# Optimization experiments

Hardware: AMD Instinct MI355X
Metric: run time of the kernel (lower is better)

Reference implementation:

```python
import jax, jax.numpy as jnp
from jax import lax
import numpy as np

I, H = 2048, 128
EPS = 1e-5


def setup_inputs() -> dict:
    key = jax.random.key(0)
    ks = jax.random.split(key, 12)
    s_ih = 1.0 / np.sqrt(H)  # torch nn.RNN init: U(-1/sqrt(H), 1/sqrt(H))
    s_fc = 1.0 / np.sqrt(H)
    u = lambda k, shape, s: jax.random.uniform(k, shape, jnp.float32, -s, s)
    return {
        "x": jax.random.normal(ks[0], (64, 512, I), jnp.float32),
        "W_ih": u(ks[1], (H, I), s_ih),
        "b_ih": u(ks[2], (H,), s_ih),
        "W_hh": u(ks[3], (H, H), s_ih),
        "b_hh": u(ks[4], (H,), s_ih),
        "W1": u(ks[5], (H, H), s_fc),
        "b1": u(ks[6], (H,), s_fc),
        "W2": u(ks[7], (H, H), s_fc),
        "b2": u(ks[8], (H,), s_fc),
        "gamma": jnp.ones((H,), jnp.float32),
        "beta": jnp.zeros((H,), jnp.float32),
    }


def reference(x, W_ih, b_ih, W_hh, b_hh, W1, b1, W2, b2, gamma, beta):
    B = x.shape[0]
    # Precompute input projection for all timesteps: [B, T, H]
    xp = jnp.einsum('bti,hi->bth', x, W_ih) + b_ih

    def step(h, xt):  # h: [B, H], xt: [B, H]
        h_new = jnp.tanh(xt + h @ W_hh.T + b_hh)
        return h_new, None

    h0 = jnp.zeros((B, H), x.dtype)
    hT, _ = lax.scan(step, h0, jnp.swapaxes(xp, 0, 1))  # scan over T

    z = jax.nn.relu(hT @ W1.T + b1)
    z = jax.nn.relu(z @ W2.T + b2)
    mu = jnp.mean(z, axis=-1, keepdims=True)
    var = jnp.mean(jnp.square(z - mu), axis=-1, keepdims=True)
    return gamma * (z - mu) * lax.rsqrt(var + EPS) + beta
```

## Files before the change

### kernel.cpp

```cpp
#include <hip/hip_runtime.h>


typedef __bf16 bf16x8 __attribute__((ext_vector_type(8)));
typedef float  f32x4  __attribute__((ext_vector_type(4)));

#define T_STEPS 512
#define I_DIM   2048
#define H_DIM   128
#define B_DIM   64
#define M_TOT   (B_DIM * T_STEPS)

__device__ __forceinline__ unsigned short f2bf(float f) {
    unsigned int u = __float_as_uint(f);
    u += 0x7FFFu + ((u >> 16) & 1u);
    return (unsigned short)(u >> 16);
}

#define BM  128
#define BK  64
#define LDK 72

__global__ __launch_bounds__(256) void gemm_xp(
    const float* __restrict__ x,
    const float* __restrict__ w,
    const float* __restrict__ b_ih,
    const float* __restrict__ b_hh,
    float* __restrict__ xp)
{
    __shared__ __align__(16) unsigned short As[BM * LDK];
    __shared__ __align__(16) unsigned short Bs[H_DIM * LDK];

    const int tid = threadIdx.x;
    const int m0  = blockIdx.x * BM;

    const int r0 = tid >> 4;
    const int c4 = tid & 15;

    const int lane = tid & 63;
    const int wave = tid >> 6;
    const int wm   = (wave >> 1) * 64;
    const int wn   = (wave & 1) * 64;
    const int l16  = lane & 15;
    const int quad = lane >> 4;

    f32x4 acc[4][4] = {};

    float4 ar[8], br[8];

    auto load_tiles = [&](int k0) {
        #pragma unroll
        for (int i = 0; i < 8; ++i)
            ar[i] = *(const float4*)(x + (size_t)(m0 + i * 16 + r0) * I_DIM + k0 + c4 * 4);
        #pragma unroll
        for (int i = 0; i < 8; ++i)
            br[i] = *(const float4*)(w + (size_t)(i * 16 + r0) * I_DIM + k0 + c4 * 4);
    };

    auto store_tiles = [&]() {
        #pragma unroll
        for (int i = 0; i < 8; ++i) {
            ushort4 v;
            v.x = f2bf(ar[i].x); v.y = f2bf(ar[i].y);
            v.z = f2bf(ar[i].z); v.w = f2bf(ar[i].w);
            *(ushort4*)(As + (i * 16 + r0) * LDK + c4 * 4) = v;
        }
        #pragma unroll
        for (int i = 0; i < 8; ++i) {
            ushort4 v;
            v.x = f2bf(br[i].x); v.y = f2bf(br[i].y);
            v.z = f2bf(br[i].z); v.w = f2bf(br[i].w);
            *(ushort4*)(Bs + (i * 16 + r0) * LDK + c4 * 4) = v;
        }
    };

    load_tiles(0);

    for (int k0 = 0; k0 < I_DIM; k0 += BK) {
        __syncthreads();
        store_tiles();
        if (k0 + BK < I_DIM) load_tiles(k0 + BK);
        __syncthreads();

        #pragma unroll
        for (int kt = 0; kt < 2; ++kt) {
            bf16x8 af[4], bfr[4];
            #pragma unroll
            for (int i = 0; i < 4; ++i)
                af[i] = *(const bf16x8*)(As + (wm + i * 16 + l16) * LDK + kt * 32 + quad * 8);
            #pragma unroll
            for (int i = 0; i < 4; ++i)
                bfr[i] = *(const bf16x8*)(Bs + (wn + i * 16 + l16) * LDK + kt * 32 + quad * 8);
            #pragma unroll
            for (int i = 0; i < 4; ++i)
                #pragma unroll
                for (int j = 0; j < 4; ++j)
                    acc[i][j] = __builtin_amdgcn_mfma_f32_16x16x32_bf16(af[i], bfr[j], acc[i][j], 0, 0, 0);
        }
    }

    #pragma unroll
    for (int j = 0; j < 4; ++j) {
        const int col  = wn + j * 16 + l16;
        const float bias = b_ih[col] + b_hh[col];
        #pragma unroll
        for (int i = 0; i < 4; ++i) {
            #pragma unroll
            for (int r = 0; r < 4; ++r) {
                const int row = wm + i * 16 + quad * 4 + r;
                xp[(size_t)(m0 + row) * H_DIM + col] = acc[i][j][r] + bias;
            }
        }
    }
}

__global__ __launch_bounds__(256) void rnn_tail(
    const float* __restrict__ xp,
    const float* __restrict__ Whh,
    const float* __restrict__ W1, const float* __restrict__ b1,
    const float* __restrict__ W2, const float* __restrict__ b2,
    const float* __restrict__ gamma, const float* __restrict__ beta,
    float* __restrict__ out)
{
    __shared__ float hs[2][H_DIM];
    __shared__ float zb[H_DIM];
    __shared__ float red[4][2];

    const int tid  = threadIdx.x;
    const int b    = blockIdx.x;
    const int j    = tid >> 1;
    const int half = tid & 1;

    float4 wr[16];
    {
        const float4* wrow = (const float4*)(Whh + j * H_DIM + half * 64);
        #pragma unroll
        for (int i = 0; i < 16; ++i) wr[i] = wrow[i];
    }

    if (tid < H_DIM) hs[0][tid] = 0.f;
    const float* xpp = xp + (size_t)b * T_STEPS * H_DIM;
    float xv = xpp[j];
    __syncthreads();

    for (int t = 0; t < T_STEPS; ++t) {
        float xnext = (t < T_STEPS - 1) ? xpp[(t + 1) * H_DIM + j] : 0.f;

        const float4* hv = (const float4*)(hs[t & 1] + half * 64);
        float p0 = 0.f, p1 = 0.f, p2 = 0.f, p3 = 0.f;
        #pragma unroll
        for (int i = 0; i < 16; i += 4) {
            float4 h0 = hv[i], h1 = hv[i + 1], h2 = hv[i + 2], h3 = hv[i + 3];
            p0 += wr[i].x     * h0.x + wr[i].y     * h0.y + wr[i].z     * h0.z + wr[i].w     * h0.w;
            p1 += wr[i + 1].x * h1.x + wr[i + 1].y * h1.y + wr[i + 1].z * h1.z + wr[i + 1].w * h1.w;
            p2 += wr[i + 2].x * h2.x + wr[i + 2].y * h2.y + wr[i + 2].z * h2.z + wr[i + 2].w * h2.w;
            p3 += wr[i + 3].x * h3.x + wr[i + 3].y * h3.y + wr[i + 3].z * h3.z + wr[i + 3].w * h3.w;
        }
        float p = (p0 + p1) + (p2 + p3);
        p += __shfl_xor(p, 1);

        float a  = xv + p;
        float e  = __expf(-2.f * fabsf(a));
        float th = (1.f - e) / (1.f + e);
        th = copysignf(th, a);

        if (half == 0) hs[(t + 1) & 1][j] = th;
        xv = xnext;
        __syncthreads();
    }

    {
        const float4* wv = (const float4*)(W1 + j * H_DIM + half * 64);
        const float4* hv = (const float4*)(hs[0] + half * 64);
        float p0 = 0.f, p1 = 0.f;
        #pragma unroll
        for (int i = 0; i < 16; i += 2) {
            float4 w0 = wv[i], w1_ = wv[i + 1], h0 = hv[i], h1 = hv[i + 1];
            p0 += w0.x * h0.x + w0.y * h0.y + w0.z * h0.z + w0.w * h0.w;
            p1 += w1_.x * h1.x + w1_.y * h1.y + w1_.z * h1.z + w1_.w * h1.w;
        }
        float p = p0 + p1;
        p += __shfl_xor(p, 1);
        float z = fmaxf(p + b1[j], 0.f);
        if (half == 0) zb[j] = z;
    }
    __syncthreads();

    {
        const float4* wv = (const float4*)(W2 + j * H_DIM + half * 64);
        const float4* zv = (const float4*)(zb + half * 64);
        float p0 = 0.f, p1 = 0.f;
        #pragma unroll
        for (int i = 0; i < 16; i += 2) {
            float4 w0 = wv[i], w1_ = wv[i + 1], z0 = zv[i], z1 = zv[i + 1];
            p0 += w0.x * z0.x + w0.y * z0.y + w0.z * z0.z + w0.w * z0.w;
            p1 += w1_.x * z1.x + w1_.y * z1.y + w1_.z * z1.z + w1_.w * z1.w;
        }
        float p = p0 + p1;
        p += __shfl_xor(p, 1);
        float z2 = fmaxf(p + b2[j], 0.f);
        if (half == 0) hs[1][j] = z2;
    }
    __syncthreads();

    float v = (tid < H_DIM) ? hs[1][tid] : 0.f;
    float s = v, q = v * v;
    #pragma unroll
    for (int o = 1; o < 64; o <<= 1) {
        s += __shfl_xor(s, o);
        q += __shfl_xor(q, o);
    }
    const int lane = tid & 63, wave = tid >> 6;
    if (lane == 0) { red[wave][0] = s; red[wave][1] = q; }
    __syncthreads();
    float S = red[0][0] + red[1][0] + red[2][0] + red[3][0];
    float Q = red[0][1] + red[1][1] + red[2][1] + red[3][1];
    float mu   = S * (1.f / 128.f);
    float var  = Q * (1.f / 128.f) - mu * mu;
    float rstd = rsqrtf(var + 1e-5f);
    if (tid < H_DIM)
        out[b * H_DIM + tid] = gamma[tid] * (v - mu) * rstd + beta[tid];
}

extern "C" void kernel_launch(void* const* d_in, const int* in_sizes, int n_in,
                              void* d_out, int out_size, void* d_ws, size_t ws_size,
                              hipStream_t stream) {
    const float* x     = (const float*)d_in[0];
    const float* W_ih  = (const float*)d_in[1];
    const float* b_ih  = (const float*)d_in[2];
    const float* W_hh  = (const float*)d_in[3];
    const float* b_hh  = (const float*)d_in[4];
    const float* W1    = (const float*)d_in[5];
    const float* b1    = (const float*)d_in[6];
    const float* W2    = (const float*)d_in[7];
    const float* b2    = (const float*)d_in[8];
    const float* gamma = (const float*)d_in[9];
    const float* beta  = (const float*)d_in[10];
    float* out = (float*)d_out;

    float* xp = (float*)d_ws;

    gemm_xp<<<dim3(M_TOT / BM), dim3(256), 0, stream>>>(x, W_ih, b_ih, b_hh, xp);
    rnn_tail<<<dim3(B_DIM), dim3(256), 0, stream>>>(xp, W_hh, W1, b1, W2, b2,
                                                    gamma, beta, out);
}
```

Measured before the change: 654.9 us.

## Batch 16 sequences per block and run recurrent matvec on bf16 MFMA

```diff
diff --git a/kernel.cpp b/kernel.cpp
--- a/kernel.cpp
+++ b/kernel.cpp
@@ -15,16 +15,27 @@
     u += 0x7FFFu + ((u >> 16) & 1u);
     return (unsigned short)(u >> 16);
 }
-
-#define BM  128
+__device__ __forceinline__ float bf2f(unsigned short u) {
+    return __uint_as_float(((unsigned int)u) << 16);
+}
+__device__ __forceinline__ bf16x8 packbf8(float4 lo, float4 hi) {
+    union { bf16x8 v; unsigned short u[8]; } r;
+    r.u[0] = f2bf(lo.x); r.u[1] = f2bf(lo.y); r.u[2] = f2bf(lo.z); r.u[3] = f2bf(lo.w);
+    r.u[4] = f2bf(hi.x); r.u[5] = f2bf(hi.y); r.u[6] = f2bf(hi.z); r.u[7] = f2bf(hi.w);
+    return r.v;
+}
+__device__ __forceinline__ float tanh_fast(float a) {
+    float q = __expf(a + a);
+    return (q - 1.f) * __builtin_amdgcn_rcpf(q + 1.f);
+}
+
+#define BM  64
 #define BK  64
 #define LDK 72
 
 __global__ __launch_bounds__(256) void gemm_xp(
-    const float* __restrict__ x,
-    const float* __restrict__ w,
-    const float* __restrict__ b_ih,
-    const float* __restrict__ b_hh,
+    const float* __restrict__ x, const float* __restrict__ w,
+    const float* __restrict__ b_ih, const float* __restrict__ b_hh,
     float* __restrict__ xp)
 {
     __shared__ __align__(16) unsigned short As[BM * LDK];
@@ -32,88 +43,79 @@
 
     const int tid = threadIdx.x;
     const int m0  = blockIdx.x * BM;
-
-    const int r0 = tid >> 4;
-    const int c4 = tid & 15;
-
-    const int lane = tid & 63;
-    const int wave = tid >> 6;
-    const int wm   = (wave >> 1) * 64;
-    const int wn   = (wave & 1) * 64;
-    const int l16  = lane & 15;
-    const int quad = lane >> 4;
-
-    f32x4 acc[4][4] = {};
-
-    float4 ar[8], br[8];
+    const int r0  = tid >> 4;
+    const int c4  = tid & 15;
+    const int lane = tid & 63, wave = tid >> 6;
+    const int wm = (wave >> 1) * 32;
+    const int wn = (wave & 1) * 64;
+    const int l16 = lane & 15, quad = lane >> 4;
+
+    f32x4 acc[2][4] = {};
+    float4 ar[4], br[8];
 
     auto load_tiles = [&](int k0) {
         #pragma unroll
-        for (int i = 0; i < 8; ++i)
+        for (int i = 0; i < 4; ++i)
             ar[i] = *(const float4*)(x + (size_t)(m0 + i * 16 + r0) * I_DIM + k0 + c4 * 4);
         #pragma unroll
         for (int i = 0; i < 8; ++i)
             br[i] = *(const float4*)(w + (size_t)(i * 16 + r0) * I_DIM + k0 + c4 * 4);
     };
-
     auto store_tiles = [&]() {
         #pragma unroll
+        for (int i = 0; i < 4; ++i) {
+            ushort4 v; v.x = f2bf(ar[i].x); v.y = f2bf(ar[i].y);
+                       v.z = f2bf(ar[i].z); v.w = f2bf(ar[i].w);
+            *(ushort4*)(As + (i * 16 + r0) * LDK + c4 * 4) = v;
+        }
+        #pragma unroll
         for (int i = 0; i < 8; ++i) {
-            ushort4 v;
-            v.x = f2bf(ar[i].x); v.y = f2bf(ar[i].y);
-            v.z = f2bf(ar[i].z); v.w = f2bf(ar[i].w);
-            *(ushort4*)(As + (i * 16 + r0) * LDK + c4 * 4) = v;
-        }
-        #pragma unroll
-        for (int i = 0; i < 8; ++i) {
-            ushort4 v;
-            v.x = f2bf(br[i].x); v.y = f2bf(br[i].y);
-            v.z = f2bf(br[i].z); v.w = f2bf(br[i].w);
+            ushort4 v; v.x = f2bf(br[i].x); v.y = f2bf(br[i].y);
+                       v.z = f2bf(br[i].z); v.w = f2bf(br[i].w);
             *(ushort4*)(Bs + (i * 16 + r0) * LDK + c4 * 4) = v;
         }
     };
 
     load_tiles(0);
-
     for (int k0 = 0; k0 < I_DIM; k0 += BK) {
         __syncthreads();
         store_tiles();
         if (k0 + BK < I_DIM) load_tiles(k0 + BK);
         __syncthreads();
-
         #pragma unroll
         for (int kt = 0; kt < 2; ++kt) {
-            bf16x8 af[4], bfr[4];
-            #pragma unroll
-            for (int i = 0; i < 4; ++i)
+            bf16x8 af[2], bfr[4];
+            #pragma unroll
+            for (int i = 0; i < 2; ++i)
                 af[i] = *(const bf16x8*)(As + (wm + i * 16 + l16) * LDK + kt * 32 + quad * 8);
             #pragma unroll
-            for (int i = 0; i < 4; ++i)
-                bfr[i] = *(const bf16x8*)(Bs + (wn + i * 16 + l16) * LDK + kt * 32 + quad * 8);
-            #pragma unroll
-            for (int i = 0; i < 4; ++i)
+            for (int j = 0; j < 4; ++j)
+                bfr[j] = *(const bf16x8*)(Bs + (wn + j * 16 + l16) * LDK + kt * 32 + quad * 8);
+            #pragma unroll
+            for (int i = 0; i < 2; ++i)
                 #pragma unroll
                 for (int j = 0; j < 4; ++j)
                     acc[i][j] = __builtin_amdgcn_mfma_f32_16x16x32_bf16(af[i], bfr[j], acc[i][j], 0, 0, 0);
         }
     }
-
     #pragma unroll
     for (int j = 0; j < 4; ++j) {
-        const int col  = wn + j * 16 + l16;
+        const int col = wn + j * 16 + l16;
         const float bias = b_ih[col] + b_hh[col];
         #pragma unroll
-        for (int i = 0; i < 4; ++i) {
+        for (int i = 0; i < 2; ++i)
             #pragma unroll
             for (int r = 0; r < 4; ++r) {
                 const int row = wm + i * 16 + quad * 4 + r;
                 xp[(size_t)(m0 + row) * H_DIM + col] = acc[i][j][r] + bias;
             }
-        }
-    }
-}
-
-__global__ __launch_bounds__(256) void rnn_tail(
+    }
+}
+
+#define NB  16
+#define LDH 136
+
+__global__ __launch_bounds__(256) void rnn_scan(
     const float* __restrict__ xp,
     const float* __restrict__ Whh,
     const float* __restrict__ W1, const float* __restrict__ b1,
@@ -121,104 +123,108 @@
     const float* __restrict__ gamma, const float* __restrict__ beta,
     float* __restrict__ out)
 {
-    __shared__ float hs[2][H_DIM];
-    __shared__ float zb[H_DIM];
-    __shared__ float red[4][2];
+    __shared__ __align__(16) unsigned short hbuf[2][NB * LDH];
+    __shared__ float ztmp[NB][129];
+    __shared__ float ztmp2[NB][129];
 
     const int tid  = threadIdx.x;
-    const int b    = blockIdx.x;
-    const int j    = tid >> 1;
-    const int half = tid & 1;
-
-    float4 wr[16];
-    {
-        const float4* wrow = (const float4*)(Whh + j * H_DIM + half * 64);
-        #pragma unroll
-        for (int i = 0; i < 16; ++i) wr[i] = wrow[i];
-    }
-
-    if (tid < H_DIM) hs[0][tid] = 0.f;
-    const float* xpp = xp + (size_t)b * T_STEPS * H_DIM;
-    float xv = xpp[j];
+    const int lane = tid & 63, w = tid >> 6;
+    const int l16  = lane & 15, quad = lane >> 4;
+    const int b0   = blockIdx.x * NB;
+
+    bf16x8 afr[2][4];
+    #pragma unroll
+    for (int t = 0; t < 2; ++t) {
+        const float* wrow = Whh + (32 * w + 16 * t + l16) * H_DIM;
+        #pragma unroll
+        for (int ks = 0; ks < 4; ++ks) {
+            float4 lo = *(const float4*)(wrow + 32 * ks + 8 * quad);
+            float4 hi = *(const float4*)(wrow + 32 * ks + 8 * quad + 4);
+            afr[t][ks] = packbf8(lo, hi);
+        }
+    }
+
+    const float* xpb = xp + (size_t)(b0 + l16) * T_STEPS * H_DIM + 32 * w + 4 * quad;
+    float4 xc0 = *(const float4*)(xpb);
+    float4 xc1 = *(const float4*)(xpb + 16);
+
+    for (int i = tid; i < NB * LDH; i += 256) hbuf[0][i] = 0;
     __syncthreads();
 
+    const f32x4 z4 = {0.f, 0.f, 0.f, 0.f};
+    const int rbase = l16 * LDH + quad * 8;
+
     for (int t = 0; t < T_STEPS; ++t) {
-        float xnext = (t < T_STEPS - 1) ? xpp[(t + 1) * H_DIM + j] : 0.f;
-
-        const float4* hv = (const float4*)(hs[t & 1] + half * 64);
-        float p0 = 0.f, p1 = 0.f, p2 = 0.f, p3 = 0.f;
-        #pragma unroll
-        for (int i = 0; i < 16; i += 4) {
-            float4 h0 = hv[i], h1 = hv[i + 1], h2 = hv[i + 2], h3 = hv[i + 3];
-            p0 += wr[i].x     * h0.x + wr[i].y     * h0.y + wr[i].z     * h0.z + wr[i].w     * h0.w;
-            p1 += wr[i + 1].x * h1.x + wr[i + 1].y * h1.y + wr[i + 1].z * h1.z + wr[i + 1].w * h1.w;
-            p2 += wr[i + 2].x * h2.x + wr[i + 2].y * h2.y + wr[i + 2].z * h2.z + wr[i + 2].w * h2.w;
-            p3 += wr[i + 3].x * h3.x + wr[i + 3].y * h3.y + wr[i + 3].z * h3.z + wr[i + 3].w * h3.w;
-        }
-        float p = (p0 + p1) + (p2 + p3);
-        p += __shfl_xor(p, 1);
-
-        float a  = xv + p;
-        float e  = __expf(-2.f * fabsf(a));
-        float th = (1.f - e) / (1.f + e);
-        th = copysignf(th, a);
-
-        if (half == 0) hs[(t + 1) & 1][j] = th;
-        xv = xnext;
+        const unsigned short* hb = hbuf[t & 1];
+        bf16x8 bf0 = *(const bf16x8*)(hb + rbase);
+        bf16x8 bf1 = *(const bf16x8*)(hb + rbase + 32);
+        bf16x8 bf2 = *(const bf16x8*)(hb + rbase + 64);
+        bf16x8 bf3 = *(const bf16x8*)(hb + rbase + 96);
+
+        const int tn = (t + 1 < T_STEPS) ? t + 1 : t;
+        float4 xn0 = *(const float4*)(xpb + (size_t)tn * H_DIM);
+        float4 xn1 = *(const float4*)(xpb + (size_t)tn * H_DIM + 16);
+
+        unsigned short* hn = hbuf[(t + 1) & 1];
+        #pragma unroll
+        for (int tl = 0; tl < 2; ++tl) {
+            f32x4 p0 = __builtin_amdgcn_mfma_f32_16x16x32_bf16(afr[tl][0], bf0, z4, 0, 0, 0);
+            p0 = __builtin_amdgcn_mfma_f32_16x16x32_bf16(afr[tl][1], bf1, p0, 0, 0, 0);
+            f32x4 p1 = __builtin_amdgcn_mfma_f32_16x16x32_bf16(afr[tl][2], bf2, z4, 0, 0, 0);
+            p1 = __builtin_amdgcn_mfma_f32_16x16x32_bf16(afr[tl][3], bf3, p1, 0, 0, 0);
+            const float4 xc = tl ? xc1 : xc0;
+            float t0 = tanh_fast(p0[0] + p1[0] + xc.x);
+            float t1 = tanh_fast(p0[1] + p1[1] + xc.y);
+            float t2 = tanh_fast(p0[2] + p1[2] + xc.z);
+            float t3 = tanh_fast(p0[3] + p1[3] + xc.w);
+            ushort4 v; v.x = f2bf(t0); v.y = f2bf(t1); v.z = f2bf(t2); v.w = f2bf(t3);
+            *(ushort4*)(hn + l16 * LDH + 32 * w + 16 * tl + 4 * quad) = v;
+        }
+        xc0 = xn0; xc1 = xn1;
         __syncthreads();
     }
 
-    {
-        const float4* wv = (const float4*)(W1 + j * H_DIM + half * 64);
-        const float4* hv = (const float4*)(hs[0] + half * 64);
-        float p0 = 0.f, p1 = 0.f;
-        #pragma unroll
-        for (int i = 0; i < 16; i += 2) {
-            float4 w0 = wv[i], w1_ = wv[i + 1], h0 = hv[i], h1 = hv[i + 1];
-            p0 += w0.x * h0.x + w0.y * h0.y + w0.z * h0.z + w0.w * h0.w;
-            p1 += w1_.x * h1.x + w1_.y * h1.y + w1_.z * h1.z + w1_.w * h1.w;
-        }
-        float p = p0 + p1;
-        p += __shfl_xor(p, 1);
-        float z = fmaxf(p + b1[j], 0.f);
-        if (half == 0) zb[j] = z;
-    }
+    const int n  = tid >> 4;
+    const int j0 = (tid & 15) * 8;
+    const unsigned short* hT = hbuf[0] + n * LDH;
+
+    float s[8];
+    #pragma unroll
+    for (int i = 0; i < 8; ++i) s[i] = b1[j0 + i];
+    for (int k = 0; k < H_DIM; ++k) {
+        float hv = bf2f(hT[k]);
+        #pragma unroll
+        for (int i = 0; i < 8; ++i) s[i] += hv * W1[(j0 + i) * H_DIM + k];
+    }
+    #pragma unroll
+    for (int i = 0; i < 8; ++i) ztmp[n][j0 + i] = fmaxf(s[i], 0.f);
     __syncthreads();
 
-    {
-        const float4* wv = (const float4*)(W2 + j * H_DIM + half * 64);
-        const float4* zv = (const float4*)(zb + half * 64);
-        float p0 = 0.f, p1 = 0.f;
-        #pragma unroll
-        for (int i = 0; i < 16; i += 2) {
-            float4 w0 = wv[i], w1_ = wv[i + 1], z0 = zv[i], z1 = zv[i + 1];
-            p0 += w0.x * z0.x + w0.y * z0.y + w0.z * z0.z + w0.w * z0.w;
-            p1 += w1_.x * z1.x + w1_.y * z1.y + w1_.z * z1.z + w1_.w * z1.w;
-        }
-        float p = p0 + p1;
-        p += __shfl_xor(p, 1);
-        float z2 = fmaxf(p + b2[j], 0.f);
-        if (half == 0) hs[1][j] = z2;
-    }
+    #pragma unroll
+    for (int i = 0; i < 8; ++i) s[i] = b2[j0 + i];
+    for (int k = 0; k < H_DIM; ++k) {
+        float zv = ztmp[n][k];
+        #pragma unroll
+        for (int i = 0; i < 8; ++i) s[i] += zv * W2[(j0 + i) * H_DIM + k];
+    }
+    #pragma unroll
+    for (int i = 0; i < 8; ++i) ztmp2[n][j0 + i] = fmaxf(s[i], 0.f);
     __syncthreads();
 
-    float v = (tid < H_DIM) ? hs[1][tid] : 0.f;
-    float s = v, q = v * v;
-    #pragma unroll
-    for (int o = 1; o < 64; o <<= 1) {
-        s += __shfl_xor(s, o);
-        q += __shfl_xor(q, o);
-    }
-    const int lane = tid & 63, wave = tid >> 6;
-    if (lane == 0) { red[wave][0] = s; red[wave][1] = q; }
-    __syncthreads();
-    float S = red[0][0] + red[1][0] + red[2][0] + red[3][0];
-    float Q = red[0][1] + red[1][1] + red[2][1] + red[3][1];
-    float mu   = S * (1.f / 128.f);
-    float var  = Q * (1.f / 128.f) - mu * mu;
+    float sum = 0.f, sq = 0.f;
+    #pragma unroll
+    for (int i = 0; i < 8; ++i) { float v = ztmp2[n][j0 + i]; sum += v; sq += v * v; }
+    #pragma unroll
+    for (int o = 1; o < 16; o <<= 1) { sum += __shfl_xor(sum, o); sq += __shfl_xor(sq, o); }
+    float mu   = sum * (1.f / 128.f);
+    float var  = sq * (1.f / 128.f) - mu * mu;
     float rstd = rsqrtf(var + 1e-5f);
-    if (tid < H_DIM)
-        out[b * H_DIM + tid] = gamma[tid] * (v - mu) * rstd + beta[tid];
+    #pragma unroll
+    for (int i = 0; i < 8; ++i) {
+        int j = j0 + i;
+        out[(size_t)(b0 + n) * H_DIM + j] =
+            gamma[j] * (ztmp2[n][j] - mu) * rstd + beta[j];
+    }
 }
 
 extern "C" void kernel_launch(void* const* d_in, const int* in_sizes, int n_in,
@@ -240,6 +246,6 @@
     float* xp = (float*)d_ws;
 
     gemm_xp<<<dim3(M_TOT / BM), dim3(256), 0, stream>>>(x, W_ih, b_ih, b_hh, xp);
-    rnn_tail<<<dim3(B_DIM), dim3(256), 0, stream>>>(xp, W_hh, W1, b1, W2, b2,
-                                                    gamma, beta, out);
-}
+    rnn_scan<<<dim3(B_DIM / NB), dim3(256), 0, stream>>>(xp, W_hh, W1, b1, W2, b2,
+                                                         gamma, beta, out);
+}
```

Measured after the change: 725.9 us. +10.8%, slower.
